# Kernel tuning notes

Hardware: AMD Instinct MI355X
Metric: run time of the kernel (lower is better)

The kernel has to match this reference:

```python
import jax, jax.numpy as jnp
import numpy as np

FEAT = 512
COND = 768
N_HEADS = 8
D_HEAD = 64
D_ATTN = N_HEADS * D_HEAD  # 512


def setup_inputs() -> dict:
    key = jax.random.key(0)
    ks = jax.random.split(key, 8)
    B, N, M = 16, 4096, 77
    x = jax.random.normal(ks[0], (B, N, FEAT), dtype=jnp.float32)
    cond = jax.random.normal(ks[1], (B, M, COND), dtype=jnp.float32)
    s_f = 1.0 / np.sqrt(FEAT)
    s_c = 1.0 / np.sqrt(COND)
    s_a = 1.0 / np.sqrt(D_ATTN)
    Wq = jax.random.normal(ks[2], (FEAT, D_ATTN), dtype=jnp.float32) * s_f
    Wk = jax.random.normal(ks[3], (COND, D_ATTN), dtype=jnp.float32) * s_c
    Wv = jax.random.normal(ks[4], (COND, D_ATTN), dtype=jnp.float32) * s_c
    Wo = jax.random.normal(ks[5], (D_ATTN, FEAT), dtype=jnp.float32) * s_a
    bo = jax.random.normal(ks[6], (FEAT,), dtype=jnp.float32) * 0.01
    return {"x": x, "cond": cond, "Wq": Wq, "Wk": Wk, "Wv": Wv, "Wo": Wo, "bo": bo}


def reference(x, cond, Wq, Wk, Wv, Wo, bo):
    B, N, _ = x.shape
    M = cond.shape[1]
    scale = D_HEAD ** (-0.5)
    # projections (no bias, as in nn.Linear(..., bias=False))
    q = (x @ Wq).reshape(B, N, N_HEADS, D_HEAD)
    k = (cond @ Wk).reshape(B, M, N_HEADS, D_HEAD)
    v = (cond @ Wv).reshape(B, M, N_HEADS, D_HEAD)
    attn = jnp.einsum('bihd,bjhd->bhij', q, k) * scale  # [B,H,N,M]
    attn = jax.nn.softmax(attn, axis=-1)  # split-half inplace softmax == plain softmax
    out = jnp.einsum('bhij,bjhd->bihd', attn, v).reshape(B, N, D_ATTN)
    return out @ Wo + bo
```

## Files before the change

kernel.cpp:

```cpp
#include <hip/hip_runtime.h>

typedef __attribute__((ext_vector_type(8))) _Float16 f16x8;
typedef __attribute__((ext_vector_type(4))) float f32x4;

#define B_SZ   16
#define N_SEQ  4096
#define M_CTX  77
#define M_PAD  96
#define NH     8

__device__ __forceinline__ _Float16 f2h(float x) { return (_Float16)x; }

__device__ __forceinline__ void gload16(const void* g, void* l) {
    __builtin_amdgcn_global_load_lds(
        (const __attribute__((address_space(1))) unsigned int*)g,
        (__attribute__((address_space(3))) unsigned int*)l, 16, 0, 0);
}

__global__ __launch_bounds__(256)
void convert(const float4* __restrict__ x, f16x8* __restrict__ xh, int n8)
{
    int idx = blockIdx.x * 256 + threadIdx.x;
    int stride = gridDim.x * 256;
    for (int i = idx; i < n8; i += stride) {
        float4 a = x[2 * i];
        float4 b = x[2 * i + 1];
        f16x8 o;
        o[0] = f2h(a.x); o[1] = f2h(a.y); o[2] = f2h(a.z); o[3] = f2h(a.w);
        o[4] = f2h(b.x); o[5] = f2h(b.y); o[6] = f2h(b.z); o[7] = f2h(b.w);
        xh[i] = o;
    }
}

__global__ __launch_bounds__(256)
void prep(const float* __restrict__ Wq, const float* __restrict__ Wk,
          const float* __restrict__ Wv, const float* __restrict__ Wo,
          _Float16* __restrict__ WqT, _Float16* __restrict__ WkT,
          _Float16* __restrict__ WvT, _Float16* __restrict__ WoT)
{
    __shared__ float t[32][33];
    const float* W; _Float16* WT; int K; float scale = 1.0f;
    switch (blockIdx.z) {
        case 0:  W = Wq; WT = WqT; K = 512; scale = 0.125f; break;
        case 1:  W = Wk; WT = WkT; K = 768; break;
        case 2:  W = Wv; WT = WvT; K = 768; break;
        default: W = Wo; WT = WoT; K = 512; break;
    }
    const int ky = blockIdx.y;
    if (ky * 32 >= K) return;
    const int nx = blockIdx.x;
    const int tr = threadIdx.x >> 5, tc = threadIdx.x & 31;
#pragma unroll
    for (int i = 0; i < 4; ++i) {
        int kr = tr + i * 8;
        t[kr][tc] = W[(size_t)(ky * 32 + kr) * 512 + nx * 32 + tc];
    }
    __syncthreads();
#pragma unroll
    for (int i = 0; i < 4; ++i) {
        int nr = tr + i * 8;
        WT[(size_t)(nx * 32 + nr) * K + ky * 32 + tc] = f2h(t[tc][nr] * scale);
    }
}

__global__ __launch_bounds__(256)
void kv_proj(const float* __restrict__ cond, const _Float16* __restrict__ WkT,
             const _Float16* __restrict__ WvT, _Float16* __restrict__ Kp,
             _Float16* __restrict__ Vt)
{
    const int tid = threadIdx.x;
    const int l = tid & 63, w = tid >> 6;
    const int lrow = l & 15, lk = l >> 4;
    const int h = blockIdx.x, b = blockIdx.y, which = blockIdx.z;
    const _Float16* WT = which ? WvT : WkT;
    const float* cb = cond + (size_t)b * M_CTX * 768;

    f32x4 acc[5];
#pragma unroll
    for (int i = 0; i < 5; ++i)
#pragma unroll
        for (int e = 0; e < 4; ++e) acc[i][e] = 0.f;

    const int n = h * 64 + w * 16 + lrow;
    for (int kk = 0; kk < 24; ++kk) {
        f16x8 bfrag = *(const f16x8*)(WT + (size_t)n * 768 + kk * 32 + lk * 8);
#pragma unroll
        for (int rt = 0; rt < 5; ++rt) {
            int m = rt * 16 + lrow;
            f16x8 afrag;
#pragma unroll
            for (int j = 0; j < 8; ++j) afrag[j] = (_Float16)0.f;
            if (m < M_CTX) {
                const float* a = cb + (size_t)m * 768 + kk * 32 + lk * 8;
                float4 f0 = *(const float4*)a;
                float4 f1 = *(const float4*)(a + 4);
                afrag[0] = f2h(f0.x); afrag[1] = f2h(f0.y);
                afrag[2] = f2h(f0.z); afrag[3] = f2h(f0.w);
                afrag[4] = f2h(f1.x); afrag[5] = f2h(f1.y);
                afrag[6] = f2h(f1.z); afrag[7] = f2h(f1.w);
            }
            acc[rt] = __builtin_amdgcn_mfma_f32_16x16x32_f16(afrag, bfrag, acc[rt], 0, 0, 0);
        }
    }

    const int bh = b * NH + h;
    const int d = w * 16 + lrow;
    if (which == 0) {
#pragma unroll
        for (int rt = 0; rt < 5; ++rt)
#pragma unroll
            for (int r = 0; r < 4; ++r) {
                int m = rt * 16 + lk * 4 + r;
                Kp[((size_t)bh * M_PAD + m) * 64 + d] = f2h(acc[rt][r]);
            }
#pragma unroll
        for (int r = 0; r < 4; ++r) {
            int m = 80 + lk * 4 + r;
            Kp[((size_t)bh * M_PAD + m) * 64 + d] = (_Float16)0.f;
        }
    } else {
#pragma unroll
        for (int rt = 0; rt < 5; ++rt)
#pragma unroll
            for (int r = 0; r < 4; ++r) {
                int m = rt * 16 + lk * 4 + r;
                Vt[((size_t)bh * 64 + d) * M_PAD + m] = f2h(acc[rt][r]);
            }
#pragma unroll
        for (int r = 0; r < 4; ++r) {
            int m = 80 + lk * 4 + r;
            Vt[((size_t)bh * 64 + d) * M_PAD + m] = (_Float16)0.f;
        }
    }
}

template<int EMODE>
__global__ __launch_bounds__(256)
void gemm512(const _Float16* __restrict__ A, const _Float16* __restrict__ BT,
             void* __restrict__ Cv, const float* __restrict__ bias)
{
    __shared__ _Float16 As[128 * 64];
    __shared__ _Float16 Bs[128 * 64];

    const int bid = blockIdx.x;
    const int wg = (bid & 7) * 256 + (bid >> 3);
    const int rb = wg >> 2;
    const int cb = wg & 3;
    const size_t row0 = (size_t)rb * 128;
    const int col0 = cb * 128;

    const int tid = threadIdx.x;
    const int l = tid & 63;
    const int w = tid >> 6;
    const int wy = w >> 1, wx = w & 1;
    const int lrow = l & 15, lk = l >> 4;

    f32x4 acc[4][4];
#pragma unroll
    for (int i = 0; i < 4; ++i)
#pragma unroll
        for (int j = 0; j < 4; ++j)
#pragma unroll
            for (int e = 0; e < 4; ++e) acc[i][j][e] = 0.f;

    const int srow_in_seg = l >> 3;
    const int sslot = (l & 7) ^ (srow_in_seg & 7);
    const _Float16* a_src0 = A + (row0 + (size_t)(w * 32 + srow_in_seg)) * 512 + sslot * 8;
    const _Float16* b_src0 = BT + ((size_t)(col0 + w * 32 + srow_in_seg)) * 512 + sslot * 8;

    for (int kt = 0; kt < 8; ++kt) {
        const _Float16* ak = a_src0 + kt * 64;
        const _Float16* bk = b_src0 + kt * 64;
#pragma unroll
        for (int s = 0; s < 4; ++s) {
            gload16(ak + (size_t)s * 8 * 512, As + (w * 4 + s) * 512);
            gload16(bk + (size_t)s * 8 * 512, Bs + (w * 4 + s) * 512);
        }
        __syncthreads();

#pragma unroll
        for (int kk = 0; kk < 2; ++kk) {
            f16x8 af[4], bf[4];
#pragma unroll
            for (int mt = 0; mt < 4; ++mt) {
                int R = wy * 64 + mt * 16 + lrow;
                int p = (kk * 4 + lk) ^ (lrow & 7);
                af[mt] = *(const f16x8*)&As[R * 64 + p * 8];
            }
#pragma unroll
            for (int nt = 0; nt < 4; ++nt) {
                int R = wx * 64 + nt * 16 + lrow;
                int p = (kk * 4 + lk) ^ (lrow & 7);
                bf[nt] = *(const f16x8*)&Bs[R * 64 + p * 8];
            }
#pragma unroll
            for (int mt = 0; mt < 4; ++mt)
#pragma unroll
                for (int nt = 0; nt < 4; ++nt)
                    acc[mt][nt] = __builtin_amdgcn_mfma_f32_16x16x32_f16(af[mt], bf[nt], acc[mt][nt], 0, 0, 0);
        }
        __syncthreads();
    }

#pragma unroll
    for (int mt = 0; mt < 4; ++mt)
#pragma unroll
        for (int nt = 0; nt < 4; ++nt)
#pragma unroll
            for (int r = 0; r < 4; ++r) {
                size_t row = row0 + wy * 64 + mt * 16 + lk * 4 + r;
                int col = col0 + wx * 64 + nt * 16 + lrow;
                float v = acc[mt][nt][r];
                if (EMODE == 0) {
                    ((_Float16*)Cv)[row * 512 + col] = f2h(v);
                } else {
                    ((float*)Cv)[row * 512 + col] = v + bias[col];
                }
            }
}

__global__ __launch_bounds__(256)
void attn(const _Float16* __restrict__ Q, const _Float16* __restrict__ Kp,
          const _Float16* __restrict__ Vt, _Float16* __restrict__ AO)
{
    __shared__ _Float16 Pl[4][16][104];
    const int tid = threadIdx.x;
    const int l = tid & 63, w = tid >> 6;
    const int lrow = l & 15, lk = l >> 4;
    const int b = blockIdx.y, tile = blockIdx.x;
    const size_t rowbase = (size_t)b * N_SEQ + tile * 64 + w * 16;

    for (int idx = l; idx < 256; idx += 64)
        Pl[w][idx >> 4][80 + (idx & 15)] = (_Float16)0.f;

    for (int h = 0; h < NH; ++h) {
        const size_t qoff = (rowbase + lrow) * 512 + h * 64;
        f16x8 qf0 = *(const f16x8*)(Q + qoff + lk * 8);
        f16x8 qf1 = *(const f16x8*)(Q + qoff + 32 + lk * 8);

        const _Float16* Kb = Kp + (size_t)(b * NH + h) * M_PAD * 64;
        f32x4 s[5];
#pragma unroll
        for (int i = 0; i < 5; ++i)
#pragma unroll
            for (int e = 0; e < 4; ++e) s[i][e] = 0.f;

#pragma unroll
        for (int ct = 0; ct < 5; ++ct) {
            f16x8 kf0 = *(const f16x8*)(Kb + (size_t)(ct * 16 + lrow) * 64 + lk * 8);
            f16x8 kf1 = *(const f16x8*)(Kb + (size_t)(ct * 16 + lrow) * 64 + 32 + lk * 8);
            s[ct] = __builtin_amdgcn_mfma_f32_16x16x32_f16(qf0, kf0, s[ct], 0, 0, 0);
            s[ct] = __builtin_amdgcn_mfma_f32_16x16x32_f16(qf1, kf1, s[ct], 0, 0, 0);
        }

        const bool m4ok = (lrow < 13);
#pragma unroll
        for (int r = 0; r < 4; ++r) {
            float v[5];
#pragma unroll
            for (int ct = 0; ct < 5; ++ct) v[ct] = s[ct][r];
            float mx = fmaxf(fmaxf(fmaxf(v[0], v[1]), fmaxf(v[2], v[3])),
                             m4ok ? v[4] : -1e30f);
#pragma unroll
            for (int off = 1; off < 16; off <<= 1)
                mx = fmaxf(mx, __shfl_xor(mx, off));
            float e[5];
            float sum = 0.f;
#pragma unroll
            for (int ct = 0; ct < 4; ++ct) { e[ct] = __expf(v[ct] - mx); sum += e[ct]; }
            e[4] = m4ok ? __expf(v[4] - mx) : 0.f;
            sum += e[4];
#pragma unroll
            for (int off = 1; off < 16; off <<= 1)
                sum += __shfl_xor(sum, off);
            float rinv = 1.0f / sum;
            int prow = lk * 4 + r;
#pragma unroll
            for (int ct = 0; ct < 5; ++ct)
                Pl[w][prow][ct * 16 + lrow] = f2h(e[ct] * rinv);
        }

        const _Float16* Vb = Vt + (size_t)(b * NH + h) * 64 * M_PAD;
        f32x4 o[4];
#pragma unroll
        for (int i = 0; i < 4; ++i)
#pragma unroll
            for (int e2 = 0; e2 < 4; ++e2) o[i][e2] = 0.f;
#pragma unroll
        for (int kk = 0; kk < 3; ++kk) {
            f16x8 pa = *(const f16x8*)&Pl[w][lrow][kk * 32 + lk * 8];
#pragma unroll
            for (int ctd = 0; ctd < 4; ++ctd) {
                f16x8 vf = *(const f16x8*)(Vb + (size_t)(ctd * 16 + lrow) * M_PAD + kk * 32 + lk * 8);
                o[ctd] = __builtin_amdgcn_mfma_f32_16x16x32_f16(pa, vf, o[ctd], 0, 0, 0);
            }
        }

#pragma unroll
        for (int ctd = 0; ctd < 4; ++ctd)
#pragma unroll
            for (int r = 0; r < 4; ++r) {
                size_t row = rowbase + lk * 4 + r;
                int col = h * 64 + ctd * 16 + lrow;
                AO[row * 512 + col] = f2h(o[ctd][r]);
            }
    }
}

extern "C" void kernel_launch(void* const* d_in, const int* in_sizes, int n_in,
                              void* d_out, int out_size, void* d_ws, size_t ws_size,
                              hipStream_t stream)
{
    (void)in_sizes; (void)n_in; (void)out_size; (void)ws_size;
    const float* x    = (const float*)d_in[0];
    const float* cond = (const float*)d_in[1];
    const float* Wq   = (const float*)d_in[2];
    const float* Wk   = (const float*)d_in[3];
    const float* Wv   = (const float*)d_in[4];
    const float* Wo   = (const float*)d_in[5];
    const float* bo   = (const float*)d_in[6];

    char* ws = (char*)d_ws;
    _Float16* WqT = (_Float16*)(ws);
    _Float16* WoT = (_Float16*)(ws + 524288);
    _Float16* WkT = (_Float16*)(ws + 1048576);
    _Float16* WvT = (_Float16*)(ws + 1835008);
    _Float16* Kp  = (_Float16*)(ws + 2621440);
    _Float16* Vt  = (_Float16*)(ws + 4194304);
    _Float16* xh  = (_Float16*)(ws + 5767168);
    _Float16* AO  = xh;
    _Float16* Q   = (_Float16*)d_out;

    prep<<<dim3(16, 24, 4), 256, 0, stream>>>(Wq, Wk, Wv, Wo, WqT, WkT, WvT, WoT);
    kv_proj<<<dim3(8, 16, 2), 256, 0, stream>>>(cond, WkT, WvT, Kp, Vt);
    convert<<<dim3(2048), 256, 0, stream>>>((const float4*)x, (f16x8*)xh, 16 * 4096 * 512 / 8);
    gemm512<0><<<dim3(2048), 256, 0, stream>>>(xh, WqT, Q, nullptr);
    attn<<<dim3(64, 16), 256, 0, stream>>>(Q, Kp, Vt, AO);
    gemm512<1><<<dim3(2048), 256, 0, stream>>>(AO, WoT, d_out, bo);
}
```

Before: 265.9 us.

## Stage swizzled K/V in LDS per head and reuse across 256-row chunks

```diff
diff --git a/kernel.cpp b/kernel.cpp
--- a/kernel.cpp
+++ b/kernel.cpp
@@ -15,6 +15,28 @@
     __builtin_amdgcn_global_load_lds(
         (const __attribute__((address_space(1))) unsigned int*)g,
         (__attribute__((address_space(3))) unsigned int*)l, 16, 0, 0);
+}
+
+template<int C>
+__device__ __forceinline__ float dppf(float x) {
+    union { float f; int i; } u, v;
+    u.f = x;
+    v.i = __builtin_amdgcn_mov_dpp(u.i, C, 0xF, 0xF, true);
+    return v.f;
+}
+__device__ __forceinline__ float rmax16(float x) {
+    x = fmaxf(x, dppf<0xB1>(x));
+    x = fmaxf(x, dppf<0x4E>(x));
+    x = fmaxf(x, dppf<0x141>(x));
+    x = fmaxf(x, dppf<0x140>(x));
+    return x;
+}
+__device__ __forceinline__ float rsum16(float x) {
+    x += dppf<0xB1>(x);
+    x += dppf<0x4E>(x);
+    x += dppf<0x141>(x);
+    x += dppf<0x140>(x);
+    return x;
 }
 
 __global__ __launch_bounds__(256)
@@ -65,8 +87,8 @@
 
 __global__ __launch_bounds__(256)
 void kv_proj(const float* __restrict__ cond, const _Float16* __restrict__ WkT,
-             const _Float16* __restrict__ WvT, _Float16* __restrict__ Kp,
-             _Float16* __restrict__ Vt)
+             const _Float16* __restrict__ WvT, _Float16* __restrict__ Kswz,
+             _Float16* __restrict__ Vswz)
 {
     const int tid = threadIdx.x;
     const int l = tid & 63, w = tid >> 6;
@@ -105,31 +127,34 @@
 
     const int bh = b * NH + h;
     const int d = w * 16 + lrow;
+    const int dhi = d >> 3, dlo = d & 7;
     if (which == 0) {
+        _Float16* Kb = Kswz + (size_t)bh * (M_PAD * 64);
 #pragma unroll
         for (int rt = 0; rt < 5; ++rt)
 #pragma unroll
             for (int r = 0; r < 4; ++r) {
                 int m = rt * 16 + lk * 4 + r;
-                Kp[((size_t)bh * M_PAD + m) * 64 + d] = f2h(acc[rt][r]);
+                Kb[m * 64 + ((dhi ^ (m & 7)) * 8) + dlo] = f2h(acc[rt][r]);
             }
 #pragma unroll
         for (int r = 0; r < 4; ++r) {
             int m = 80 + lk * 4 + r;
-            Kp[((size_t)bh * M_PAD + m) * 64 + d] = (_Float16)0.f;
+            Kb[m * 64 + ((dhi ^ (m & 7)) * 8) + dlo] = (_Float16)0.f;
         }
     } else {
+        _Float16* Vb = Vswz + (size_t)bh * (64 * 128);
 #pragma unroll
         for (int rt = 0; rt < 5; ++rt)
 #pragma unroll
             for (int r = 0; r < 4; ++r) {
                 int m = rt * 16 + lk * 4 + r;
-                Vt[((size_t)bh * 64 + d) * M_PAD + m] = f2h(acc[rt][r]);
+                Vb[d * 128 + (((m >> 3) ^ dlo) * 8) + (m & 7)] = f2h(acc[rt][r]);
             }
 #pragma unroll
         for (int r = 0; r < 4; ++r) {
             int m = 80 + lk * 4 + r;
-            Vt[((size_t)bh * 64 + d) * M_PAD + m] = (_Float16)0.f;
+            Vb[d * 128 + (((m >> 3) ^ dlo) * 8) + (m & 7)] = (_Float16)0.f;
         }
     }
 }
@@ -220,67 +245,89 @@
 }
 
 __global__ __launch_bounds__(256)
-void attn(const _Float16* __restrict__ Q, const _Float16* __restrict__ Kp,
-          const _Float16* __restrict__ Vt, _Float16* __restrict__ AO)
-{
+void attn(const _Float16* __restrict__ Q, const _Float16* __restrict__ Kswz,
+          const _Float16* __restrict__ Vswz, _Float16* __restrict__ AO)
+{
+    __shared__ _Float16 Ks[M_PAD * 64];
+    __shared__ _Float16 Vs[64 * 128];
     __shared__ _Float16 Pl[4][16][104];
+
     const int tid = threadIdx.x;
     const int l = tid & 63, w = tid >> 6;
     const int lrow = l & 15, lk = l >> 4;
-    const int b = blockIdx.y, tile = blockIdx.x;
-    const size_t rowbase = (size_t)b * N_SEQ + tile * 64 + w * 16;
+    const int chunk = blockIdx.x, h = blockIdx.y, b = blockIdx.z;
+    const int bh = b * NH + h;
+
+    {
+        const _Float16* Kg = Kswz + (size_t)bh * (M_PAD * 64);
+        const _Float16* Vg = Vswz + (size_t)bh * (64 * 128);
+#pragma unroll
+        for (int i = 0; i < 3; ++i) {
+            int c = w * 3 + i;
+            gload16(Kg + c * 512 + l * 8, Ks + c * 512);
+        }
+#pragma unroll
+        for (int i = 0; i < 4; ++i) {
+            int c = w * 4 + i;
+            gload16(Vg + c * 512 + l * 8, Vs + c * 512);
+        }
+    }
+
+    const size_t row0 = (size_t)b * N_SEQ + chunk * 256 + w * 64;
+    f16x8 af[4][2];
+    {
+        const _Float16* Qb = Q + (row0 + lrow) * 512 + h * 64 + lk * 8;
+#pragma unroll
+        for (int mt = 0; mt < 4; ++mt)
+#pragma unroll
+            for (int kk = 0; kk < 2; ++kk)
+                af[mt][kk] = *(const f16x8*)(Qb + (size_t)mt * 16 * 512 + kk * 32);
+    }
 
     for (int idx = l; idx < 256; idx += 64)
         Pl[w][idx >> 4][80 + (idx & 15)] = (_Float16)0.f;
 
-    for (int h = 0; h < NH; ++h) {
-        const size_t qoff = (rowbase + lrow) * 512 + h * 64;
-        f16x8 qf0 = *(const f16x8*)(Q + qoff + lk * 8);
-        f16x8 qf1 = *(const f16x8*)(Q + qoff + 32 + lk * 8);
-
-        const _Float16* Kb = Kp + (size_t)(b * NH + h) * M_PAD * 64;
+    __syncthreads();
+
+    const bool m4ok = (lrow < 13);
+    const int kswz = lrow & 7;
+
+#pragma unroll
+    for (int mt = 0; mt < 4; ++mt) {
         f32x4 s[5];
 #pragma unroll
         for (int i = 0; i < 5; ++i)
 #pragma unroll
             for (int e = 0; e < 4; ++e) s[i][e] = 0.f;
-
-#pragma unroll
-        for (int ct = 0; ct < 5; ++ct) {
-            f16x8 kf0 = *(const f16x8*)(Kb + (size_t)(ct * 16 + lrow) * 64 + lk * 8);
-            f16x8 kf1 = *(const f16x8*)(Kb + (size_t)(ct * 16 + lrow) * 64 + 32 + lk * 8);
-            s[ct] = __builtin_amdgcn_mfma_f32_16x16x32_f16(qf0, kf0, s[ct], 0, 0, 0);
-            s[ct] = __builtin_amdgcn_mfma_f32_16x16x32_f16(qf1, kf1, s[ct], 0, 0, 0);
-        }
-
-        const bool m4ok = (lrow < 13);
+#pragma unroll
+        for (int kk = 0; kk < 2; ++kk)
+#pragma unroll
+            for (int ct = 0; ct < 5; ++ct) {
+                f16x8 kf = *(const f16x8*)&Ks[(ct * 16 + lrow) * 64 + (((kk * 4 + lk) ^ kswz) * 8)];
+                s[ct] = __builtin_amdgcn_mfma_f32_16x16x32_f16(af[mt][kk], kf, s[ct], 0, 0, 0);
+            }
+
+        float rinv[4];
 #pragma unroll
         for (int r = 0; r < 4; ++r) {
-            float v[5];
-#pragma unroll
-            for (int ct = 0; ct < 5; ++ct) v[ct] = s[ct][r];
-            float mx = fmaxf(fmaxf(fmaxf(v[0], v[1]), fmaxf(v[2], v[3])),
-                             m4ok ? v[4] : -1e30f);
-#pragma unroll
-            for (int off = 1; off < 16; off <<= 1)
-                mx = fmaxf(mx, __shfl_xor(mx, off));
-            float e[5];
-            float sum = 0.f;
-#pragma unroll
-            for (int ct = 0; ct < 4; ++ct) { e[ct] = __expf(v[ct] - mx); sum += e[ct]; }
-            e[4] = m4ok ? __expf(v[4] - mx) : 0.f;
-            sum += e[4];
-#pragma unroll
-            for (int off = 1; off < 16; off <<= 1)
-                sum += __shfl_xor(sum, off);
-            float rinv = 1.0f / sum;
+            float v0 = s[0][r], v1 = s[1][r], v2 = s[2][r], v3 = s[3][r], v4 = s[4][r];
+            float mx = fmaxf(fmaxf(v0, v1), fmaxf(v2, v3));
+            mx = fmaxf(mx, m4ok ? v4 : -1e30f);
+            mx = rmax16(mx);
+            float e0 = __expf(v0 - mx), e1 = __expf(v1 - mx);
+            float e2 = __expf(v2 - mx), e3 = __expf(v3 - mx);
+            float e4 = m4ok ? __expf(v4 - mx) : 0.f;
+            float sum = ((e0 + e1) + (e2 + e3)) + e4;
+            sum = rsum16(sum);
+            rinv[r] = 1.0f / sum;
             int prow = lk * 4 + r;
-#pragma unroll
-            for (int ct = 0; ct < 5; ++ct)
-                Pl[w][prow][ct * 16 + lrow] = f2h(e[ct] * rinv);
-        }
-
-        const _Float16* Vb = Vt + (size_t)(b * NH + h) * 64 * M_PAD;
+            Pl[w][prow][lrow]      = f2h(e0);
+            Pl[w][prow][16 + lrow] = f2h(e1);
+            Pl[w][prow][32 + lrow] = f2h(e2);
+            Pl[w][prow][48 + lrow] = f2h(e3);
+            Pl[w][prow][64 + lrow] = f2h(e4);
+        }
+
         f32x4 o[4];
 #pragma unroll
         for (int i = 0; i < 4; ++i)
@@ -291,19 +338,17 @@
             f16x8 pa = *(const f16x8*)&Pl[w][lrow][kk * 32 + lk * 8];
 #pragma unroll
             for (int ctd = 0; ctd < 4; ++ctd) {
-                f16x8 vf = *(const f16x8*)(Vb + (size_t)(ctd * 16 + lrow) * M_PAD + kk * 32 + lk * 8);
+                f16x8 vf = *(const f16x8*)&Vs[(ctd * 16 + lrow) * 128 + (((kk * 4 + lk) ^ kswz) * 8)];
                 o[ctd] = __builtin_amdgcn_mfma_f32_16x16x32_f16(pa, vf, o[ctd], 0, 0, 0);
             }
         }
 
+        const size_t rw = row0 + mt * 16 + lk * 4;
 #pragma unroll
         for (int ctd = 0; ctd < 4; ++ctd)
 #pragma unroll
-            for (int r = 0; r < 4; ++r) {
-                size_t row = rowbase + lk * 4 + r;
-                int col = h * 64 + ctd * 16 + lrow;
-                AO[row * 512 + col] = f2h(o[ctd][r]);
-            }
+            for (int r = 0; r < 4; ++r)
+                AO[(rw + r) * 512 + h * 64 + ctd * 16 + lrow] = f2h(o[ctd][r] * rinv[r]);
     }
 }
 
@@ -321,20 +366,20 @@
     const float* bo   = (const float*)d_in[6];
 
     char* ws = (char*)d_ws;
-    _Float16* WqT = (_Float16*)(ws);
-    _Float16* WoT = (_Float16*)(ws + 524288);
-    _Float16* WkT = (_Float16*)(ws + 1048576);
-    _Float16* WvT = (_Float16*)(ws + 1835008);
-    _Float16* Kp  = (_Float16*)(ws + 2621440);
-    _Float16* Vt  = (_Float16*)(ws + 4194304);
-    _Float16* xh  = (_Float16*)(ws + 5767168);
-    _Float16* AO  = xh;
-    _Float16* Q   = (_Float16*)d_out;
+    _Float16* WqT  = (_Float16*)(ws);
+    _Float16* WoT  = (_Float16*)(ws + 524288);
+    _Float16* Kswz = (_Float16*)(ws + 1048576);
+    _Float16* Vswz = (_Float16*)(ws + 2621440);
+    _Float16* xh   = (_Float16*)(ws + 4718592);
+    _Float16* WkT  = (_Float16*)(ws + 4718592);
+    _Float16* WvT  = (_Float16*)(ws + 4718592 + 786432);
+    _Float16* AO   = xh;
+    _Float16* Qf   = (_Float16*)d_out;
 
     prep<<<dim3(16, 24, 4), 256, 0, stream>>>(Wq, Wk, Wv, Wo, WqT, WkT, WvT, WoT);
-    kv_proj<<<dim3(8, 16, 2), 256, 0, stream>>>(cond, WkT, WvT, Kp, Vt);
+    kv_proj<<<dim3(8, 16, 2), 256, 0, stream>>>(cond, WkT, WvT, Kswz, Vswz);
     convert<<<dim3(2048), 256, 0, stream>>>((const float4*)x, (f16x8*)xh, 16 * 4096 * 512 / 8);
-    gemm512<0><<<dim3(2048), 256, 0, stream>>>(xh, WqT, Q, nullptr);
-    attn<<<dim3(64, 16), 256, 0, stream>>>(Q, Kp, Vt, AO);
+    gemm512<0><<<dim3(2048), 256, 0, stream>>>(xh, WqT, Qf, nullptr);
+    attn<<<dim3(16, 8, 16), 256, 0, stream>>>(Qf, Kswz, Vswz, AO);
     gemm512<1><<<dim3(2048), 256, 0, stream>>>(AO, WoT, d_out, bo);
 }
```

After: 228.1 us. 14.2% less time.
